# Kernel optimization log

Measured on AMD Instinct MI355X. Metric: run time of the kernel, lower is better.

## Reference

```python
import jax, jax.numpy as jnp
import numpy as np

N, IN_DIM, E_RAW, N_GRAPHS, HEADS = 50000, 128, 800000, 256, 2
NEG_ATT, NEG_ACT, EPS = 0.2, 0.01, 1e-5


def _gat(x, src, dst, W, a_src, a_dst, bias):
    # PyG GATConv: x' = xW per head; alpha = softmax_over_dst(leaky_relu(a_s.h_src + a_d.h_dst, 0.2))
    H, C = a_src.shape
    n = x.shape[0]
    h = (x @ W).reshape(n, H, C)                                  # [N,H,C]
    al_s = jnp.einsum('nhc,hc->nh', h, a_src)                     # [N,H]
    al_d = jnp.einsum('nhc,hc->nh', h, a_dst)                     # [N,H]
    e = jax.nn.leaky_relu(al_s[src] + al_d[dst], NEG_ATT)         # [E,H]
    m = jax.ops.segment_max(e, dst, num_segments=n)               # per-dst max (stable softmax)
    ee = jnp.exp(e - m[dst])
    s = jax.ops.segment_sum(ee, dst, num_segments=n)
    alpha = ee / (s[dst] + 1e-16)                                 # [E,H]
    out = jax.ops.segment_sum(h[src] * alpha[:, :, None], dst, num_segments=n)
    return out.reshape(n, H * C) + bias


def _bn(x, g, b):
    # training-mode BatchNorm1d over nodes (biased variance), eps=1e-5
    m = jnp.mean(x, 0)
    v = jnp.var(x, 0)
    return (x - m) * jax.lax.rsqrt(v + EPS) * g + b


def setup_inputs() -> dict:
    key = jax.random.key(0)
    ks = jax.random.split(key, 20)
    H, C1, C2, C3 = HEADS, 32, 64, 128
    rn = lambda i, sh, s=0.05: jax.random.normal(ks[i], sh, jnp.float32) * s
    inp = dict(
        x=jax.random.normal(ks[0], (N, IN_DIM), jnp.float32),
        edge_index=jax.random.randint(ks[1], (2, E_RAW), 0, N, jnp.int32),
        edge_weigth=jax.random.uniform(ks[2], (E_RAW,), jnp.float32),
        batch=jnp.sort(jax.random.randint(ks[3], (N,), 0, N_GRAPHS, jnp.int32)),
        W1=rn(4, (IN_DIM, H * C1)), a_src1=rn(5, (H, C1)), a_dst1=rn(6, (H, C1)),
        b1=jnp.zeros((H * C1,), jnp.float32), g1=jnp.ones((H * C1,), jnp.float32), be1=jnp.zeros((H * C1,), jnp.float32),
        W2=rn(7, (H * C1, H * C2)), a_src2=rn(8, (H, C2)), a_dst2=rn(9, (H, C2)),
        b2=jnp.zeros((H * C2,), jnp.float32), g2=jnp.ones((H * C2,), jnp.float32), be2=jnp.zeros((H * C2,), jnp.float32),
        W3=rn(10, (H * C2, H * C3)), a_src3=rn(11, (H, C3)), a_dst3=rn(12, (H, C3)),
        b3=jnp.zeros((H * C3,), jnp.float32), g3=jnp.ones((H * C3,), jnp.float32), be3=jnp.zeros((H * C3,), jnp.float32),
        Wc1=rn(13, (H * C1 + H * C2 + H * C3, 128)), bc1=jnp.zeros((128,), jnp.float32),
        Wc2=rn(14, (128, 64)), bc2=jnp.zeros((64,), jnp.float32),
        Wc3=rn(15, (64, 2)), bc3=jnp.zeros((2,), jnp.float32),
    )
    return inp


def reference(x, edge_index, edge_weigth, batch,
              W1, a_src1, a_dst1, b1, g1, be1,
              W2, a_src2, a_dst2, b2, g2, be2,
              W3, a_src3, a_dst3, b3, g3, be3,
              Wc1, bc1, Wc2, bc2, Wc3, bc3):
    n = x.shape[0]
    loops = jnp.arange(n, dtype=edge_index.dtype)  # GATConv add_self_loops=True
    src = jnp.concatenate([edge_index[0], loops])
    dst = jnp.concatenate([edge_index[1], loops])
    lr = lambda t: jax.nn.leaky_relu(t, NEG_ACT)
    x1 = lr(_bn(_gat(x, src, dst, W1, a_src1, a_dst1, b1), g1, be1))
    x2 = lr(_bn(_gat(x1, src, dst, W2, a_src2, a_dst2, b2), g2, be2))
    x3 = lr(_bn(_gat(x2, src, dst, W3, a_src3, a_dst3, b3), g3, be3))
    p = jnp.concatenate([
        jax.ops.segment_sum(x1, batch, num_segments=N_GRAPHS),
        jax.ops.segment_sum(x2, batch, num_segments=N_GRAPHS),
        jax.ops.segment_sum(x3, batch, num_segments=N_GRAPHS)], axis=1)
    h = lr(p @ Wc1 + bc1)
    h = lr(h @ Wc2 + bc2)
    return h @ Wc3 + bc3
```

## Files before the change

kernel.cpp:

```cpp
#include <hip/hip_runtime.h>
#include <hip/hip_fp16.h>
#include <math.h>

#define N_NODES 50000
#define E_RAW_N 800000
#define E_TOT   (E_RAW_N + N_NODES)
#define NGRAPH  256
#define POOL_F  448
#define SCAN_B  196
#define NSLICE  4

using f16x8 = __attribute__((ext_vector_type(8))) _Float16;
using f32x4 = __attribute__((ext_vector_type(4))) float;


template<int K, int F>
__device__ void do_wt(const float* __restrict__ W, __half* __restrict__ WT, int blk) {
    int i = blk * 256 + threadIdx.x;
    if (i >= F * (K / 8)) return;
    int f = i / (K / 8);
    int kb = (i % (K / 8)) * 8;
    __half tmp[8];
#pragma unroll
    for (int j = 0; j < 8; ++j) tmp[j] = __float2half(W[(size_t)(kb + j) * F + f]);
    *reinterpret_cast<uint4*>(WT + (size_t)f * K + kb) = *reinterpret_cast<uint4*>(tmp);
}


__global__ void k_init(int* __restrict__ deg, int* __restrict__ cursor,
                       float* __restrict__ p, float* __restrict__ bn,
                       const float* __restrict__ W1, const float* __restrict__ W2,
                       const float* __restrict__ W3, __half* __restrict__ WT1,
                       __half* __restrict__ WT2, __half* __restrict__ WT3) {
    int b = blockIdx.x;
    if (b < 448) {
        int i = b * 256 + threadIdx.x;
        if (i < N_NODES) { deg[i] = 0; cursor[i] = 0; }
        if (i < NGRAPH * POOL_F) p[i] = 0.f;
        if (i < NSLICE * 512 * 3) bn[i] = 0.f;
    } else {
        int wb = b - 448;
        if (wb < 4)       do_wt<128, 64>(W1, WT1, wb);
        else if (wb < 8)  do_wt<64, 128>(W2, WT2, wb - 4);
        else              do_wt<128, 256>(W3, WT3, wb - 8);
    }
}


__global__ void k_deg(const int* __restrict__ dst_raw, int* __restrict__ deg) {
    int e = blockIdx.x * blockDim.x + threadIdx.x;
    if (e >= E_TOT) return;
    int d = (e < E_RAW_N) ? dst_raw[e] : (e - E_RAW_N);
    atomicAdd(&deg[d], 1);
}

__global__ void k_scan1(const int* __restrict__ deg, int* __restrict__ bsum) {
    __shared__ int red[256];
    int i = blockIdx.x * 256 + threadIdx.x;
    int v = (i < N_NODES) ? deg[i] : 0;
    red[threadIdx.x] = v;
    __syncthreads();
    for (int o = 128; o > 0; o >>= 1) {
        if (threadIdx.x < o) red[threadIdx.x] += red[threadIdx.x + o];
        __syncthreads();
    }
    if (threadIdx.x == 0) bsum[blockIdx.x] = red[0];
}

__global__ void k_scan3(const int* __restrict__ deg, const int* __restrict__ bsum,
                        int* __restrict__ rowstart) {
    __shared__ int pre[256];
    __shared__ int s[256];
    int tid = threadIdx.x;
    pre[tid] = (tid < (int)blockIdx.x) ? bsum[tid] : 0;
    int i = blockIdx.x * 256 + tid;
    int v = (i < N_NODES) ? deg[i] : 0;
    s[tid] = v;
    __syncthreads();
    for (int o = 128; o > 0; o >>= 1) {
        if (tid < o) pre[tid] += pre[tid + o];
        __syncthreads();
    }
    for (int o = 1; o < 256; o <<= 1) {
        int t = (tid >= o) ? s[tid - o] : 0;
        __syncthreads();
        s[tid] += t;
        __syncthreads();
    }
    if (i < N_NODES) rowstart[i] = pre[0] + s[tid] - v;
    if (i == 0) rowstart[N_NODES] = E_TOT;
}

__global__ void k_fill(const int* __restrict__ ei, const int* __restrict__ rowstart,
                       int* __restrict__ cursor, int* __restrict__ adj) {
    int e = blockIdx.x * blockDim.x + threadIdx.x;
    if (e >= E_TOT) return;
    int s, d;
    if (e < E_RAW_N) { s = ei[e]; d = ei[E_RAW_N + e]; }
    else             { s = d = e - E_RAW_N; }
    int pos = rowstart[d] + atomicAdd(&cursor[d], 1);
    adj[pos] = s;
}


template<int K, int F, bool BNIN, typename TIN, typename TOUT>
__global__ void __launch_bounds__(256) k_mfma(
        const TIN* __restrict__ x, const __half* __restrict__ WT,
        const float* __restrict__ bnP,
        const float* __restrict__ g, const float* __restrict__ be,
        const float* __restrict__ a_src, const float* __restrict__ a_dst,
        void* __restrict__ hout, float* __restrict__ al_s, float* __restrict__ al_d) {
    constexpr int NF = F / 16;
    constexpr int KS = K / 32;
    constexpr int MT = 2;
    __shared__ float scs[K], bbs[K];
    int tid = threadIdx.x;
    if constexpr (BNIN) {
        const float invN = 1.f / (float)N_NODES;
        for (int i = tid; i < K; i += 256) {
            float sm = 0.f, sq = 0.f;
#pragma unroll
            for (int s = 0; s < NSLICE; ++s) {
                sm += bnP[s * 2 * K + i];
                sq += bnP[s * 2 * K + K + i];
            }
            float mean = sm * invN;
            float var  = sq * invN - mean * mean;
            float sc = rsqrtf(var + 1e-5f) * g[i];
            scs[i] = sc;
            bbs[i] = be[i] - mean * sc;
        }
        __syncthreads();
    }
    int wave = tid >> 6, lane = tid & 63;
    int col = lane & 15;
    int kg  = lane >> 4;
    long n_base = ((long)blockIdx.x * 4 + wave) * (MT * 16);
    if (n_base >= N_NODES) return;

    bool mv[MT];
#pragma unroll
    for (int m = 0; m < MT; ++m) mv[m] = (n_base + m * 16) < N_NODES;

    f32x4 acc[MT][NF];
#pragma unroll
    for (int m = 0; m < MT; ++m)
#pragma unroll
        for (int t = 0; t < NF; ++t) acc[m][t] = (f32x4){0.f, 0.f, 0.f, 0.f};

    for (int ks = 0; ks < KS; ++ks) {
        int kb = ks * 32 + kg * 8;
        f16x8 af[MT];
#pragma unroll
        for (int m = 0; m < MT; ++m) {
            if (!mv[m]) { af[m] = (f16x8){}; continue; }
            long nrow = n_base + m * 16 + col;
            if constexpr (sizeof(TIN) == 2) {
                uint4 u = *reinterpret_cast<const uint4*>((const __half*)x + nrow * K + kb);
                if constexpr (BNIN) {
                    const __half* hp = reinterpret_cast<const __half*>(&u);
                    f16x8 a;
#pragma unroll
                    for (int j = 0; j < 8; ++j) {
                        float y = __half2float(hp[j]) * scs[kb + j] + bbs[kb + j];
                        y = y > 0.f ? y : 0.01f * y;
                        a[j] = (_Float16)y;
                    }
                    af[m] = a;
                } else {
                    af[m] = *reinterpret_cast<const f16x8*>(&u);
                }
            } else {
                const float* xp = (const float*)x + nrow * K + kb;
                float4 v0 = *reinterpret_cast<const float4*>(xp);
                float4 v1 = *reinterpret_cast<const float4*>(xp + 4);
                f16x8 a;
                a[0] = (_Float16)v0.x; a[1] = (_Float16)v0.y;
                a[2] = (_Float16)v0.z; a[3] = (_Float16)v0.w;
                a[4] = (_Float16)v1.x; a[5] = (_Float16)v1.y;
                a[6] = (_Float16)v1.z; a[7] = (_Float16)v1.w;
                af[m] = a;
            }
        }
#pragma unroll
        for (int t = 0; t < NF; ++t) {
            f16x8 bf = *reinterpret_cast<const f16x8*>(WT + (size_t)(t * 16 + col) * K + kb);
            acc[0][t] = __builtin_amdgcn_mfma_f32_16x16x32_f16(af[0], bf, acc[0][t], 0, 0, 0);
            if constexpr (MT > 1)
                acc[1][t] = __builtin_amdgcn_mfma_f32_16x16x32_f16(af[1], bf, acc[1][t], 0, 0, 0);
        }
    }

#pragma unroll
    for (int m = 0; m < MT; ++m) {
        if (!mv[m]) continue;
#pragma unroll
        for (int t = 0; t < NF; ++t) {
#pragma unroll
            for (int r = 0; r < 4; ++r) {
                long n = n_base + m * 16 + kg * 4 + r;
                float v = acc[m][t][r];
                if constexpr (sizeof(TOUT) == 1) {
                    int pk = __builtin_amdgcn_cvt_pk_fp8_f32(v, v, 0, false);
                    reinterpret_cast<unsigned char*>(hout)[n * F + t * 16 + col] =
                        (unsigned char)(pk & 0xff);
                } else {
                    reinterpret_cast<__half*>(hout)[n * F + t * 16 + col] = __float2half(v);
                }
            }
        }
#pragma unroll
        for (int r = 0; r < 4; ++r) {
            float ss0 = 0.f, sd0 = 0.f, ss1 = 0.f, sd1 = 0.f;
#pragma unroll
            for (int t = 0; t < NF; ++t) {
                float v = acc[m][t][r];
                float as = a_src[t * 16 + col];
                float ad = a_dst[t * 16 + col];
                if (t < NF / 2) { ss0 += v * as; sd0 += v * ad; }
                else            { ss1 += v * as; sd1 += v * ad; }
            }
#pragma unroll
            for (int o = 1; o < 16; o <<= 1) {
                ss0 += __shfl_xor(ss0, o); sd0 += __shfl_xor(sd0, o);
                ss1 += __shfl_xor(ss1, o); sd1 += __shfl_xor(sd1, o);
            }
            if (col == 0) {
                long n = n_base + m * 16 + kg * 4 + r;
                al_s[n * 2]     = ss0; al_s[n * 2 + 1] = ss1;
                al_d[n * 2]     = sd0; al_d[n * 2 + 1] = sd1;
            }
        }
    }
}


template<bool FP8> struct PayT;
template<> struct PayT<false> { using T = uint4; };
template<> struct PayT<true>  { using T = uint2; };

template<bool FP8>
__device__ inline void accum8(typename PayT<FP8>::T u, float ee, float acc[8]) {
    if constexpr (FP8) {
        auto f0 = __builtin_amdgcn_cvt_pk_f32_fp8(u.x, false);
        auto f1 = __builtin_amdgcn_cvt_pk_f32_fp8(u.x, true);
        auto f2 = __builtin_amdgcn_cvt_pk_f32_fp8(u.y, false);
        auto f3 = __builtin_amdgcn_cvt_pk_f32_fp8(u.y, true);
        acc[0] += ee * f0[0]; acc[1] += ee * f0[1];
        acc[2] += ee * f1[0]; acc[3] += ee * f1[1];
        acc[4] += ee * f2[0]; acc[5] += ee * f2[1];
        acc[6] += ee * f3[0]; acc[7] += ee * f3[1];
    } else {
        float2 f0 = __half22float2(*reinterpret_cast<const __half2*>(&u.x));
        float2 f1 = __half22float2(*reinterpret_cast<const __half2*>(&u.y));
        float2 f2 = __half22float2(*reinterpret_cast<const __half2*>(&u.z));
        float2 f3 = __half22float2(*reinterpret_cast<const __half2*>(&u.w));
        acc[0] += ee * f0.x; acc[1] += ee * f0.y;
        acc[2] += ee * f1.x; acc[3] += ee * f1.y;
        acc[4] += ee * f2.x; acc[5] += ee * f2.y;
        acc[6] += ee * f3.x; acc[7] += ee * f3.y;
    }
}

template<int F, int C, bool FP8>
__global__ void __launch_bounds__(256) k_gather(
        const int* __restrict__ rowstart, const int* __restrict__ adj,
        const void* __restrict__ hv, const float* __restrict__ al_s,
        const float* __restrict__ al_d, const float* __restrict__ bias,
        __half* __restrict__ xpre) {
    using LT = typename PayT<FP8>::T;
    constexpr int HPL = 8;
    constexpr int LPE = F / HPL;
    constexpr int EPI = 64 / LPE;
    constexpr int UNR = (EPI >= 8) ? 4 : (16 / EPI);
    constexpr int STEP = UNR * EPI;
    constexpr int EB  = FP8 ? 1 : 2;
    int wave = (blockIdx.x * 256 + threadIdx.x) >> 6;
    int lane = threadIdx.x & 63;
    if (wave >= N_NODES) return;
    int n = wave;
    int rs = rowstart[n], re = rowstart[n + 1];
    float2 aldv = *reinterpret_cast<const float2*>(al_d + n * 2);

    const int es = lane / LPE;
    const int fl = lane % LPE;
    const int fi = fl * HPL;
    const int hd = (fi >= C) ? 1 : 0;
    const float alh = hd ? aldv.y : aldv.x;
    const char* base = (const char*)hv;

    float acc[HPL];
#pragma unroll
    for (int j = 0; j < HPL; ++j) acc[j] = 0.f;
    float seh = 0.f;

    int nsteps = (re - rs + STEP - 1) / STEP;
    int sN[UNR];
#pragma unroll
    for (int u = 0; u < UNR; ++u) {
        int e = rs + u * EPI + es;
        sN[u] = adj[min(e, re - 1)];
    }
    for (int t = 0; t < nsteps; ++t) {
        int ibase = rs + t * STEP;
        int sC[UNR];
#pragma unroll
        for (int u = 0; u < UNR; ++u) sC[u] = sN[u];
        if (t + 1 < nsteps) {
            int nb = ibase + STEP;
#pragma unroll
            for (int u = 0; u < UNR; ++u) {
                int e = nb + u * EPI + es;
                sN[u] = adj[min(e, re - 1)];
            }
        }
        float alsN[UNR];
        LT hvN[UNR];
#pragma unroll
        for (int u = 0; u < UNR; ++u) {
            alsN[u] = al_s[sC[u] * 2 + hd];
            hvN[u] = *reinterpret_cast<const LT*>(base + (size_t)sC[u] * F * EB + fi * EB);
        }
#pragma unroll
        for (int u = 0; u < UNR; ++u) {
            bool valid = (ibase + u * EPI + es) < re;
            float v = alsN[u] + alh; v = v > 0.f ? v : 0.2f * v;
            v = fminf(v, 80.f);
            float ee = valid ? __expf(v) : 0.f;
            seh += ee;
            accum8<FP8>(hvN[u], ee, acc);
        }
    }

#pragma unroll
    for (int o = LPE; o < 64; o <<= 1) {
        seh += __shfl_xor(seh, o);
#pragma unroll
        for (int j = 0; j < HPL; ++j) acc[j] += __shfl_xor(acc[j], o);
    }

    if (es == 0) {
        float inv = 1.f / (seh + 1e-16f);
        const float* bp = bias + fi;
        __half2 o0 = __floats2half2_rn(acc[0] * inv + bp[0], acc[1] * inv + bp[1]);
        __half2 o1 = __floats2half2_rn(acc[2] * inv + bp[2], acc[3] * inv + bp[3]);
        __half2 o2 = __floats2half2_rn(acc[4] * inv + bp[4], acc[5] * inv + bp[5]);
        __half2 o3 = __floats2half2_rn(acc[6] * inv + bp[6], acc[7] * inv + bp[7]);
        uint4 u;
        u.x = *reinterpret_cast<unsigned int*>(&o0);
        u.y = *reinterpret_cast<unsigned int*>(&o1);
        u.z = *reinterpret_cast<unsigned int*>(&o2);
        u.w = *reinterpret_cast<unsigned int*>(&o3);
        *reinterpret_cast<uint4*>(xpre + (size_t)n * F + fi) = u;
    }
}


template<int F>
__global__ void __launch_bounds__(256) k_bnstats(const __half* __restrict__ x,
        float* __restrict__ bnP) {
    constexpr int SLOTS = F / 8;
    constexpr int RPI   = 256 / SLOTS;
    __shared__ float ls[256][8];
    int tid = threadIdx.x;
    int slot = tid % SLOTS;
    int r0 = tid / SLOTS;
    int slice = blockIdx.x & (NSLICE - 1);
    float s[8], q[8];
#pragma unroll
    for (int j = 0; j < 8; ++j) { s[j] = 0.f; q[j] = 0.f; }
    int stride = gridDim.x * RPI;
    for (int n = blockIdx.x * RPI + r0; n < N_NODES; n += stride) {
        uint4 u = *reinterpret_cast<const uint4*>(x + (size_t)n * F + slot * 8);
        float2 f0 = __half22float2(*reinterpret_cast<__half2*>(&u.x));
        float2 f1 = __half22float2(*reinterpret_cast<__half2*>(&u.y));
        float2 f2 = __half22float2(*reinterpret_cast<__half2*>(&u.z));
        float2 f3 = __half22float2(*reinterpret_cast<__half2*>(&u.w));
        float v[8] = {f0.x, f0.y, f1.x, f1.y, f2.x, f2.y, f3.x, f3.y};
#pragma unroll
        for (int j = 0; j < 8; ++j) { s[j] += v[j]; q[j] += v[j] * v[j]; }
    }
#pragma unroll
    for (int j = 0; j < 8; ++j) ls[tid][j] = s[j];
    __syncthreads();
    if (tid < F) {
        int sl = tid / 8, j = tid % 8;
        float t = 0.f;
        for (int r = 0; r < RPI; ++r) t += ls[r * SLOTS + sl][j];
        atomicAdd(&bnP[slice * 2 * F + tid], t);
    }
    __syncthreads();
#pragma unroll
    for (int j = 0; j < 8; ++j) ls[tid][j] = q[j];
    __syncthreads();
    if (tid < F) {
        int sl = tid / 8, j = tid % 8;
        float t = 0.f;
        for (int r = 0; r < RPI; ++r) t += ls[r * SLOTS + sl][j];
        atomicAdd(&bnP[slice * 2 * F + F + tid], t);
    }
}


template<int F>
__global__ void k_bnpool(const __half* __restrict__ x, const float* __restrict__ bnP,
                         const float* __restrict__ g,
                         const float* __restrict__ be, const int* __restrict__ batch,
                         float* __restrict__ p, int poff) {
    constexpr int F2 = F / 2;
    constexpr int NGRP = 512 / F;
    constexpr int NPB = 128;
    int f2 = threadIdx.x % F2;
    int grp = threadIdx.x / F2;
    int f = 2 * f2;
    const float invN = 1.f / (float)N_NODES;
    float sm0 = 0.f, sm1 = 0.f, sq0 = 0.f, sq1 = 0.f;
#pragma unroll
    for (int s = 0; s < NSLICE; ++s) {
        sm0 += bnP[s * 2 * F + f];     sm1 += bnP[s * 2 * F + f + 1];
        sq0 += bnP[s * 2 * F + F + f]; sq1 += bnP[s * 2 * F + F + f + 1];
    }
    float m0 = sm0 * invN, m1 = sm1 * invN;
    float v0 = sq0 * invN - m0 * m0;
    float v1 = sq1 * invN - m1 * m1;
    float sc0 = rsqrtf(v0 + 1e-5f) * g[f];
    float sc1 = rsqrtf(v1 + 1e-5f) * g[f + 1];
    float bb0 = be[f] - m0 * sc0;
    float bb1 = be[f + 1] - m1 * sc1;
    int n0 = blockIdx.x * NPB;
    int nend = n0 + NPB; if (nend > N_NODES) nend = N_NODES;
    int n = n0 + grp;
    if (n >= nend) return;
    float p0 = 0.f, p1 = 0.f;
    int cg = batch[n];
    for (; n < nend; n += NGRP) {
        float2 xv = __half22float2(*reinterpret_cast<const __half2*>(x + (size_t)n * F + f));
        float y0 = xv.x * sc0 + bb0; y0 = y0 > 0.f ? y0 : 0.01f * y0;
        float y1 = xv.y * sc1 + bb1; y1 = y1 > 0.f ? y1 : 0.01f * y1;
        int bg = batch[n];
        if (bg != cg) {
            atomicAdd(&p[cg * POOL_F + poff + f], p0);
            atomicAdd(&p[cg * POOL_F + poff + f + 1], p1);
            p0 = p1 = 0.f; cg = bg;
        }
        p0 += y0; p1 += y1;
    }
    atomicAdd(&p[cg * POOL_F + poff + f], p0);
    atomicAdd(&p[cg * POOL_F + poff + f + 1], p1);
}


__global__ void k_mlp(const float* __restrict__ p, const float* __restrict__ Wc1,
                      const float* __restrict__ bc1, const float* __restrict__ Wc2,
                      const float* __restrict__ bc2, const float* __restrict__ Wc3,
                      const float* __restrict__ bc3, float* __restrict__ out) {
    __shared__ float pr[POOL_F];
    __shared__ float h1[128];
    __shared__ float h2[64];
    int g = blockIdx.x, tid = threadIdx.x;
    for (int i = tid; i < POOL_F; i += 128) pr[i] = p[g * POOL_F + i];
    __syncthreads();
    float a = bc1[tid];
    for (int k = 0; k < POOL_F; ++k) a += pr[k] * Wc1[k * 128 + tid];
    a = a > 0.f ? a : 0.01f * a;
    h1[tid] = a;
    __syncthreads();
    if (tid < 64) {
        float b = bc2[tid];
        for (int k = 0; k < 128; ++k) b += h1[k] * Wc2[k * 64 + tid];
        b = b > 0.f ? b : 0.01f * b;
        h2[tid] = b;
    }
    __syncthreads();
    if (tid < 2) {
        float c = bc3[tid];
        for (int k = 0; k < 64; ++k) c += h2[k] * Wc3[k * 2 + tid];
        out[g * 2 + tid] = c;
    }
}


extern "C" void kernel_launch(void* const* d_in, const int* in_sizes, int n_in,
                              void* d_out, int out_size, void* d_ws, size_t ws_size,
                              hipStream_t stream) {
    const float* x    = (const float*)d_in[0];
    const int*   ei   = (const int*)d_in[1];
    const int*   batch= (const int*)d_in[3];
    const float* W1  = (const float*)d_in[4];
    const float* as1 = (const float*)d_in[5];
    const float* ad1 = (const float*)d_in[6];
    const float* b1  = (const float*)d_in[7];
    const float* g1  = (const float*)d_in[8];
    const float* be1 = (const float*)d_in[9];
    const float* W2  = (const float*)d_in[10];
    const float* as2 = (const float*)d_in[11];
    const float* ad2 = (const float*)d_in[12];
    const float* b2  = (const float*)d_in[13];
    const float* g2  = (const float*)d_in[14];
    const float* be2 = (const float*)d_in[15];
    const float* W3  = (const float*)d_in[16];
    const float* as3 = (const float*)d_in[17];
    const float* ad3 = (const float*)d_in[18];
    const float* b3  = (const float*)d_in[19];
    const float* g3  = (const float*)d_in[20];
    const float* be3 = (const float*)d_in[21];
    const float* Wc1 = (const float*)d_in[22];
    const float* bc1 = (const float*)d_in[23];
    const float* Wc2 = (const float*)d_in[24];
    const float* bc2 = (const float*)d_in[25];
    const float* Wc3 = (const float*)d_in[26];
    const float* bc3 = (const float*)d_in[27];
    float* out = (float*)d_out;

    char* wsb = (char*)d_ws;
    size_t off = 0;
    auto alloc = [&](size_t b) -> void* {
        void* pp = wsb + off;
        off += (b + 255) & ~(size_t)255;
        return pp;
    };
    int*    adj      = (int*)alloc((size_t)E_TOT * 4);
    int*    rowstart = (int*)alloc((size_t)(N_NODES + 1) * 4);
    int*    deg      = (int*)alloc((size_t)N_NODES * 4);
    int*    cursor   = (int*)alloc((size_t)N_NODES * 4);
    int*    bsum     = (int*)alloc(256 * 4);
    float*  al_s     = (float*)alloc((size_t)N_NODES * 2 * 4);
    float*  al_d     = (float*)alloc((size_t)N_NODES * 2 * 4);
    float*  bn1      = (float*)alloc(NSLICE * 512 * 4);
    float*  bn2      = (float*)alloc(NSLICE * 512 * 4);
    float*  bn3      = (float*)alloc(NSLICE * 512 * 4);
    float*  p        = (float*)alloc((size_t)NGRAPH * POOL_F * 4);
    __half* WT1      = (__half*)alloc((size_t)64 * 128 * 2);
    __half* WT2      = (__half*)alloc((size_t)128 * 64 * 2);
    __half* WT3      = (__half*)alloc((size_t)256 * 128 * 2);
    __half* hbuf     = (__half*)alloc((size_t)N_NODES * 128 * 2);
    unsigned char* h8buf = (unsigned char*)alloc((size_t)N_NODES * 256);
    __half* xbuf     = (__half*)alloc((size_t)N_NODES * 256 * 2);

    k_init<<<472, 256, 0, stream>>>(deg, cursor, p, bn1, W1, W2, W3, WT1, WT2, WT3);

    int eb = (E_TOT + 255) / 256;
    k_deg<<<eb, 256, 0, stream>>>(ei + E_RAW_N, deg);
    k_scan1<<<SCAN_B, 256, 0, stream>>>(deg, bsum);
    k_scan3<<<SCAN_B, 256, 0, stream>>>(deg, bsum, rowstart);
    k_fill<<<eb, 256, 0, stream>>>(ei, rowstart, cursor, adj);

    int wb = (N_NODES + 3) / 4;
    int bb = (N_NODES + 127) / 128;
    const int sb = 480;
    const int mb = 391;

    k_mfma<128, 64, false, float, __half><<<mb, 256, 0, stream>>>(
        x, WT1, nullptr, nullptr, nullptr, as1, ad1, hbuf, al_s, al_d);
    k_gather<64, 32, false><<<wb, 256, 0, stream>>>(rowstart, adj, hbuf, al_s, al_d, b1, xbuf);
    k_bnstats<64><<<sb, 256, 0, stream>>>(xbuf, bn1);
    k_bnpool<64><<<bb, 256, 0, stream>>>(xbuf, bn1, g1, be1, batch, p, 0);

    k_mfma<64, 128, true, __half, __half><<<mb, 256, 0, stream>>>(
        xbuf, WT2, bn1, g1, be1, as2, ad2, hbuf, al_s, al_d);
    k_gather<128, 64, false><<<wb, 256, 0, stream>>>(rowstart, adj, hbuf, al_s, al_d, b2, xbuf);
    k_bnstats<128><<<sb, 256, 0, stream>>>(xbuf, bn2);
    k_bnpool<128><<<bb, 256, 0, stream>>>(xbuf, bn2, g2, be2, batch, p, 64);

    k_mfma<128, 256, true, __half, unsigned char><<<mb, 256, 0, stream>>>(
        xbuf, WT3, bn2, g2, be2, as3, ad3, h8buf, al_s, al_d);
    k_gather<256, 128, true><<<wb, 256, 0, stream>>>(rowstart, adj, h8buf, al_s, al_d, b3, xbuf);
    k_bnstats<256><<<sb, 256, 0, stream>>>(xbuf, bn3);
    k_bnpool<256><<<bb, 256, 0, stream>>>(xbuf, bn3, g3, be3, batch, p, 192);

    k_mlp<<<NGRAPH, 128, 0, stream>>>(p, Wc1, bc1, Wc2, bc2, Wc3, bc3, out);
}
```

Measured before the change: 337.9 us.

## Fuse degree counting and BN-pool into MFMA launches, record per-edge rank

The degree-counting kernel is folded into the first projection launch as extra blocks. Each edge's atomic return value is stored as its rank, so the CSR fill no longer needs a second atomic pass through a cursor array. The layer-1 and layer-2 BN+pool kernels run as extra blocks of the next layer's MFMA launch, which reads the same xbuf, and the gather addressing switches to 32-bit shift-based offsets. Together this cuts the number of kernel launches and the atomic traffic, at the cost of an extra 3.4 MB rank buffer and heterogeneous blocks within one launch.

```diff
diff --git a/kernel.cpp b/kernel.cpp
--- a/kernel.cpp
+++ b/kernel.cpp
@@ -9,6 +9,9 @@
 #define POOL_F  448
 #define SCAN_B  196
 #define NSLICE  4
+#define MBLK    391
+#define EBLK    3321
+#define PBLK    391
 
 using f16x8 = __attribute__((ext_vector_type(8))) _Float16;
 using f32x4 = __attribute__((ext_vector_type(4))) float;
@@ -27,15 +30,15 @@
 }
 
 
-__global__ void k_init(int* __restrict__ deg, int* __restrict__ cursor,
-                       float* __restrict__ p, float* __restrict__ bn,
+__global__ void k_init(int* __restrict__ deg, float* __restrict__ p,
+                       float* __restrict__ bn,
                        const float* __restrict__ W1, const float* __restrict__ W2,
                        const float* __restrict__ W3, __half* __restrict__ WT1,
                        __half* __restrict__ WT2, __half* __restrict__ WT3) {
     int b = blockIdx.x;
     if (b < 448) {
         int i = b * 256 + threadIdx.x;
-        if (i < N_NODES) { deg[i] = 0; cursor[i] = 0; }
+        if (i < N_NODES) deg[i] = 0;
         if (i < NGRAPH * POOL_F) p[i] = 0.f;
         if (i < NSLICE * 512 * 3) bn[i] = 0.f;
     } else {
@@ -47,11 +50,12 @@
 }
 
 
-__global__ void k_deg(const int* __restrict__ dst_raw, int* __restrict__ deg) {
-    int e = blockIdx.x * blockDim.x + threadIdx.x;
+__device__ inline void degrank_body(int bid, const int* __restrict__ dst_raw,
+                                    int* __restrict__ deg, int* __restrict__ rank) {
+    int e = bid * 256 + threadIdx.x;
     if (e >= E_TOT) return;
     int d = (e < E_RAW_N) ? dst_raw[e] : (e - E_RAW_N);
-    atomicAdd(&deg[d], 1);
+    rank[e] = atomicAdd(&deg[d], 1);
 }
 
 __global__ void k_scan1(const int* __restrict__ deg, int* __restrict__ bsum) {
@@ -92,24 +96,88 @@
 }
 
 __global__ void k_fill(const int* __restrict__ ei, const int* __restrict__ rowstart,
-                       int* __restrict__ cursor, int* __restrict__ adj) {
+                       const int* __restrict__ rank, int* __restrict__ adj) {
     int e = blockIdx.x * blockDim.x + threadIdx.x;
     if (e >= E_TOT) return;
     int s, d;
     if (e < E_RAW_N) { s = ei[e]; d = ei[E_RAW_N + e]; }
     else             { s = d = e - E_RAW_N; }
-    int pos = rowstart[d] + atomicAdd(&cursor[d], 1);
-    adj[pos] = s;
-}
-
-
-template<int K, int F, bool BNIN, typename TIN, typename TOUT>
+    adj[rowstart[d] + rank[e]] = s;
+}
+
+
+template<int F>
+__device__ void bnpool_body(int bid, const __half* __restrict__ x,
+                            const float* __restrict__ bnP, const float* __restrict__ g,
+                            const float* __restrict__ be, const int* __restrict__ batch,
+                            float* __restrict__ p, int poff) {
+    constexpr int F2 = F / 2;
+    constexpr int NGRP = 512 / F;
+    constexpr int NPB = 128;
+    int f2 = threadIdx.x % F2;
+    int grp = threadIdx.x / F2;
+    int f = 2 * f2;
+    const float invN = 1.f / (float)N_NODES;
+    float sm0 = 0.f, sm1 = 0.f, sq0 = 0.f, sq1 = 0.f;
+#pragma unroll
+    for (int s = 0; s < NSLICE; ++s) {
+        sm0 += bnP[s * 2 * F + f];     sm1 += bnP[s * 2 * F + f + 1];
+        sq0 += bnP[s * 2 * F + F + f]; sq1 += bnP[s * 2 * F + F + f + 1];
+    }
+    float m0 = sm0 * invN, m1 = sm1 * invN;
+    float v0 = sq0 * invN - m0 * m0;
+    float v1 = sq1 * invN - m1 * m1;
+    float sc0 = rsqrtf(v0 + 1e-5f) * g[f];
+    float sc1 = rsqrtf(v1 + 1e-5f) * g[f + 1];
+    float bb0 = be[f] - m0 * sc0;
+    float bb1 = be[f + 1] - m1 * sc1;
+    int n0 = bid * NPB;
+    int nend = n0 + NPB; if (nend > N_NODES) nend = N_NODES;
+    int n = n0 + grp;
+    if (n >= nend) return;
+    float p0 = 0.f, p1 = 0.f;
+    int cg = batch[n];
+    for (; n < nend; n += NGRP) {
+        float2 xv = __half22float2(*reinterpret_cast<const __half2*>(x + (size_t)n * F + f));
+        float y0 = xv.x * sc0 + bb0; y0 = y0 > 0.f ? y0 : 0.01f * y0;
+        float y1 = xv.y * sc1 + bb1; y1 = y1 > 0.f ? y1 : 0.01f * y1;
+        int bg = batch[n];
+        if (bg != cg) {
+            atomicAdd(&p[cg * POOL_F + poff + f], p0);
+            atomicAdd(&p[cg * POOL_F + poff + f + 1], p1);
+            p0 = p1 = 0.f; cg = bg;
+        }
+        p0 += y0; p1 += y1;
+    }
+    atomicAdd(&p[cg * POOL_F + poff + f], p0);
+    atomicAdd(&p[cg * POOL_F + poff + f + 1], p1);
+}
+
+template<int F>
+__global__ void k_bnpool(const __half* __restrict__ x, const float* __restrict__ bnP,
+                         const float* __restrict__ g, const float* __restrict__ be,
+                         const int* __restrict__ batch, float* __restrict__ p, int poff) {
+    bnpool_body<F>(blockIdx.x, x, bnP, g, be, batch, p, poff);
+}
+
+
+template<int K, int F, bool BNIN, typename TIN, typename TOUT, int SIDE>
 __global__ void __launch_bounds__(256) k_mfma(
         const TIN* __restrict__ x, const __half* __restrict__ WT,
         const float* __restrict__ bnP,
         const float* __restrict__ g, const float* __restrict__ be,
         const float* __restrict__ a_src, const float* __restrict__ a_dst,
-        void* __restrict__ hout, float* __restrict__ al_s, float* __restrict__ al_d) {
+        void* __restrict__ hout, float* __restrict__ al_s, float* __restrict__ al_d,
+        const int* __restrict__ dst_raw, int* __restrict__ deg, int* __restrict__ rank,
+        const int* __restrict__ batch, float* __restrict__ pp, int poff) {
+    if constexpr (SIDE == 1) {
+        if (blockIdx.x >= MBLK) { degrank_body(blockIdx.x - MBLK, dst_raw, deg, rank); return; }
+    } else if constexpr (SIDE == 2) {
+        if (blockIdx.x >= MBLK) {
+            bnpool_body<K>(blockIdx.x - MBLK, (const __half*)x, bnP, g, be, batch, pp, poff);
+            return;
+        }
+    }
     constexpr int NF = F / 16;
     constexpr int KS = K / 32;
     constexpr int MT = 2;
@@ -274,7 +342,7 @@
     constexpr int EPI = 64 / LPE;
     constexpr int UNR = (EPI >= 8) ? 4 : (16 / EPI);
     constexpr int STEP = UNR * EPI;
-    constexpr int EB  = FP8 ? 1 : 2;
+    constexpr unsigned RSH = FP8 ? 8 : ((F == 64) ? 7 : 8);
     int wave = (blockIdx.x * 256 + threadIdx.x) >> 6;
     int lane = threadIdx.x & 63;
     if (wave >= N_NODES) return;
@@ -284,10 +352,12 @@
 
     const int es = lane / LPE;
     const int fl = lane % LPE;
-    const int fi = fl * HPL;
+    const unsigned fi = fl * HPL;
     const int hd = (fi >= C) ? 1 : 0;
     const float alh = hd ? aldv.y : aldv.x;
     const char* base = (const char*)hv;
+    const char* alsb = (const char*)al_s;
+    const unsigned fioff = FP8 ? fi : fi * 2;
 
     float acc[HPL];
 #pragma unroll
@@ -295,15 +365,15 @@
     float seh = 0.f;
 
     int nsteps = (re - rs + STEP - 1) / STEP;
-    int sN[UNR];
+    unsigned sN[UNR];
 #pragma unroll
     for (int u = 0; u < UNR; ++u) {
         int e = rs + u * EPI + es;
-        sN[u] = adj[min(e, re - 1)];
+        sN[u] = (unsigned)adj[min(e, re - 1)];
     }
     for (int t = 0; t < nsteps; ++t) {
         int ibase = rs + t * STEP;
-        int sC[UNR];
+        unsigned sC[UNR];
 #pragma unroll
         for (int u = 0; u < UNR; ++u) sC[u] = sN[u];
         if (t + 1 < nsteps) {
@@ -311,15 +381,15 @@
 #pragma unroll
             for (int u = 0; u < UNR; ++u) {
                 int e = nb + u * EPI + es;
-                sN[u] = adj[min(e, re - 1)];
+                sN[u] = (unsigned)adj[min(e, re - 1)];
             }
         }
         float alsN[UNR];
         LT hvN[UNR];
 #pragma unroll
         for (int u = 0; u < UNR; ++u) {
-            alsN[u] = al_s[sC[u] * 2 + hd];
-            hvN[u] = *reinterpret_cast<const LT*>(base + (size_t)sC[u] * F * EB + fi * EB);
+            alsN[u] = *reinterpret_cast<const float*>(alsb + ((sC[u] << 3) | (unsigned)(hd << 2)));
+            hvN[u] = *reinterpret_cast<const LT*>(base + ((sC[u] << RSH) + fioff));
         }
 #pragma unroll
         for (int u = 0; u < UNR; ++u) {
@@ -399,54 +469,6 @@
         for (int r = 0; r < RPI; ++r) t += ls[r * SLOTS + sl][j];
         atomicAdd(&bnP[slice * 2 * F + F + tid], t);
     }
-}
-
-
-template<int F>
-__global__ void k_bnpool(const __half* __restrict__ x, const float* __restrict__ bnP,
-                         const float* __restrict__ g,
-                         const float* __restrict__ be, const int* __restrict__ batch,
-                         float* __restrict__ p, int poff) {
-    constexpr int F2 = F / 2;
-    constexpr int NGRP = 512 / F;
-    constexpr int NPB = 128;
-    int f2 = threadIdx.x % F2;
-    int grp = threadIdx.x / F2;
-    int f = 2 * f2;
-    const float invN = 1.f / (float)N_NODES;
-    float sm0 = 0.f, sm1 = 0.f, sq0 = 0.f, sq1 = 0.f;
-#pragma unroll
-    for (int s = 0; s < NSLICE; ++s) {
-        sm0 += bnP[s * 2 * F + f];     sm1 += bnP[s * 2 * F + f + 1];
-        sq0 += bnP[s * 2 * F + F + f]; sq1 += bnP[s * 2 * F + F + f + 1];
-    }
-    float m0 = sm0 * invN, m1 = sm1 * invN;
-    float v0 = sq0 * invN - m0 * m0;
-    float v1 = sq1 * invN - m1 * m1;
-    float sc0 = rsqrtf(v0 + 1e-5f) * g[f];
-    float sc1 = rsqrtf(v1 + 1e-5f) * g[f + 1];
-    float bb0 = be[f] - m0 * sc0;
-    float bb1 = be[f + 1] - m1 * sc1;
-    int n0 = blockIdx.x * NPB;
-    int nend = n0 + NPB; if (nend > N_NODES) nend = N_NODES;
-    int n = n0 + grp;
-    if (n >= nend) return;
-    float p0 = 0.f, p1 = 0.f;
-    int cg = batch[n];
-    for (; n < nend; n += NGRP) {
-        float2 xv = __half22float2(*reinterpret_cast<const __half2*>(x + (size_t)n * F + f));
-        float y0 = xv.x * sc0 + bb0; y0 = y0 > 0.f ? y0 : 0.01f * y0;
-        float y1 = xv.y * sc1 + bb1; y1 = y1 > 0.f ? y1 : 0.01f * y1;
-        int bg = batch[n];
-        if (bg != cg) {
-            atomicAdd(&p[cg * POOL_F + poff + f], p0);
-            atomicAdd(&p[cg * POOL_F + poff + f + 1], p1);
-            p0 = p1 = 0.f; cg = bg;
-        }
-        p0 += y0; p1 += y1;
-    }
-    atomicAdd(&p[cg * POOL_F + poff + f], p0);
-    atomicAdd(&p[cg * POOL_F + poff + f + 1], p1);
 }
 
 
@@ -520,9 +542,9 @@
         return pp;
     };
     int*    adj      = (int*)alloc((size_t)E_TOT * 4);
+    int*    rank     = (int*)alloc((size_t)E_TOT * 4);
     int*    rowstart = (int*)alloc((size_t)(N_NODES + 1) * 4);
     int*    deg      = (int*)alloc((size_t)N_NODES * 4);
-    int*    cursor   = (int*)alloc((size_t)N_NODES * 4);
     int*    bsum     = (int*)alloc(256 * 4);
     float*  al_s     = (float*)alloc((size_t)N_NODES * 2 * 4);
     float*  al_d     = (float*)alloc((size_t)N_NODES * 2 * 4);
@@ -537,36 +559,33 @@
     unsigned char* h8buf = (unsigned char*)alloc((size_t)N_NODES * 256);
     __half* xbuf     = (__half*)alloc((size_t)N_NODES * 256 * 2);
 
-    k_init<<<472, 256, 0, stream>>>(deg, cursor, p, bn1, W1, W2, W3, WT1, WT2, WT3);
-
-    int eb = (E_TOT + 255) / 256;
-    k_deg<<<eb, 256, 0, stream>>>(ei + E_RAW_N, deg);
+    k_init<<<472, 256, 0, stream>>>(deg, p, bn1, W1, W2, W3, WT1, WT2, WT3);
+
+    int wb = (N_NODES + 3) / 4;
+    const int sb = 480;
+
+    k_mfma<128, 64, false, float, __half, 1><<<MBLK + EBLK, 256, 0, stream>>>(
+        x, WT1, nullptr, nullptr, nullptr, as1, ad1, hbuf, al_s, al_d,
+        ei + E_RAW_N, deg, rank, nullptr, nullptr, 0);
     k_scan1<<<SCAN_B, 256, 0, stream>>>(deg, bsum);
     k_scan3<<<SCAN_B, 256, 0, stream>>>(deg, bsum, rowstart);
-    k_fill<<<eb, 256, 0, stream>>>(ei, rowstart, cursor, adj);
-
-    int wb = (N_NODES + 3) / 4;
-    int bb = (N_NODES + 127) / 128;
-    const int sb = 480;
-    const int mb = 391;
-
-    k_mfma<128, 64, false, float, __half><<<mb, 256, 0, stream>>>(
-        x, WT1, nullptr, nullptr, nullptr, as1, ad1, hbuf, al_s, al_d);
+    k_fill<<<EBLK, 256, 0, stream>>>(ei, rowstart, rank, adj);
+
     k_gather<64, 32, false><<<wb, 256, 0, stream>>>(rowstart, adj, hbuf, al_s, al_d, b1, xbuf);
     k_bnstats<64><<<sb, 256, 0, stream>>>(xbuf, bn1);
-    k_bnpool<64><<<bb, 256, 0, stream>>>(xbuf, bn1, g1, be1, batch, p, 0);
-
-    k_mfma<64, 128, true, __half, __half><<<mb, 256, 0, stream>>>(
-        xbuf, WT2, bn1, g1, be1, as2, ad2, hbuf, al_s, al_d);
+
+    k_mfma<64, 128, true, __half, __half, 2><<<MBLK + PBLK, 256, 0, stream>>>(
+        xbuf, WT2, bn1, g1, be1, as2, ad2, hbuf, al_s, al_d,
+        nullptr, nullptr, nullptr, batch, p, 0);
     k_gather<128, 64, false><<<wb, 256, 0, stream>>>(rowstart, adj, hbuf, al_s, al_d, b2, xbuf);
     k_bnstats<128><<<sb, 256, 0, stream>>>(xbuf, bn2);
-    k_bnpool<128><<<bb, 256, 0, stream>>>(xbuf, bn2, g2, be2, batch, p, 64);
-
-    k_mfma<128, 256, true, __half, unsigned char><<<mb, 256, 0, stream>>>(
-        xbuf, WT3, bn2, g2, be2, as3, ad3, h8buf, al_s, al_d);
+
+    k_mfma<128, 256, true, __half, unsigned char, 2><<<MBLK + PBLK, 256, 0, stream>>>(
+        xbuf, WT3, bn2, g2, be2, as3, ad3, h8buf, al_s, al_d,
+        nullptr, nullptr, nullptr, batch, p, 64);
     k_gather<256, 128, true><<<wb, 256, 0, stream>>>(rowstart, adj, h8buf, al_s, al_d, b3, xbuf);
     k_bnstats<256><<<sb, 256, 0, stream>>>(xbuf, bn3);
-    k_bnpool<256><<<bb, 256, 0, stream>>>(xbuf, bn3, g3, be3, batch, p, 192);
-
+
+    k_bnpool<256><<<PBLK, 256, 0, stream>>>(xbuf, bn3, g3, be3, batch, p, 192);
     k_mlp<<<NGRAPH, 128, 0, stream>>>(p, Wc1, bc1, Wc2, bc2, Wc3, bc3, out);
 }
```

Result: faster. 291.2 us (-13.8%).
